# Kernel tuning notes

Measured on AMD Instinct MI355X. Metric: run time of the kernel, lower is better.

The kernel has to match this reference:

```python
import jax, jax.numpy as jnp
import numpy as np

N = 1024
C_LOCAL = 384
C_PAIR = 128
HEADS = 8
KEY_SIZE = 32
LN_EPS = 1e-5


def setup_inputs() -> dict:
    key = jax.random.key(0)
    ks = jax.random.split(key, 5)
    local = jax.random.normal(ks[0], (N, C_LOCAL), dtype=jnp.float32)
    pair = jax.random.normal(ks[1], (N, N, C_PAIR), dtype=jnp.float32)
    mask = jnp.ones((N,), dtype=bool)
    ln_scale = jnp.ones((C_LOCAL,), dtype=jnp.float32)
    ln_offset = jnp.zeros((C_LOCAL,), dtype=jnp.float32)
    W_value = jax.random.normal(ks[2], (C_LOCAL, HEADS * KEY_SIZE), dtype=jnp.float32) * (1.0 / np.sqrt(C_LOCAL))
    W_attn = jax.random.normal(ks[3], (C_PAIR, HEADS), dtype=jnp.float32) * (1.0 / np.sqrt(C_PAIR))
    W_out = jax.random.normal(ks[4], (HEADS * KEY_SIZE, C_LOCAL), dtype=jnp.float32) * (1.0 / np.sqrt(HEADS * KEY_SIZE))
    return {"local": local, "pair": pair, "mask": mask,
            "ln_scale": ln_scale, "ln_offset": ln_offset,
            "W_value": W_value, "W_attn": W_attn, "W_out": W_out}


def reference(local, pair, mask, ln_scale, ln_offset, W_value, W_attn, W_out):
    # pair_mask[i, j] = mask[i] & mask[j]
    pair_mask = (mask[:, None] & mask[None, :])[..., None]  # [N, N, 1]

    # LayerNorm over last axis (create_scale=True, create_offset=True)
    mu = jnp.mean(local, axis=-1, keepdims=True)
    var = jnp.var(local, axis=-1, keepdims=True)
    local_ln = (local - mu) * jax.lax.rsqrt(var + LN_EPS) * ln_scale + ln_offset

    # value projection -> [N, heads, key_size]
    value = (local_ln @ W_value).reshape(local.shape[0], HEADS, KEY_SIZE)

    # pair-bias attention logits -> [N, N, heads]
    attn = pair @ W_attn
    attn = jnp.where(pair_mask, attn, -1e9)
    attn = jax.nn.softmax(attn, axis=1)
    attn = jnp.where(pair_mask, attn, 0.0)

    # weighted average over j, per head -> [N, heads, key_size] -> [N, heads*key_size]
    out = jnp.einsum('ijh,jhc->ihc', attn, value).reshape(local.shape[0], -1)
    return out @ W_out
```

## Files before the change

### kernel.cpp

```cpp
#include <hip/hip_runtime.h>
#include <cstddef>

#define NN 1024
#define CL 384
#define CP 128
#define NH 8
#define KS 32
#define HK 256

typedef float floatx4 __attribute__((ext_vector_type(4)));

template<int CTRL>
__device__ __forceinline__ float dpp_mov(float v) {
    return __int_as_float(__builtin_amdgcn_update_dpp(
        0, __float_as_int(v), CTRL, 0xF, 0xF, true));
}

__device__ __forceinline__ float4 ntload4(const float* p) {
    floatx4 t = __builtin_nontemporal_load((const floatx4*)p);
    float4 r; r.x = t.x; r.y = t.y; r.z = t.z; r.w = t.w;
    return r;
}

__global__ __launch_bounds__(256) void k_ln_value(
    const float* __restrict__ local_, const float* __restrict__ ln_scale,
    const float* __restrict__ ln_offset, const float* __restrict__ Wv,
    float* __restrict__ value)
{
    __shared__ float ln_s[4][CL];
    const int tid = threadIdx.x;
    const int w = tid >> 6, lane = tid & 63;
    const int r = blockIdx.x * 4 + w;
    const float* lp = local_ + (size_t)r * CL;
    float x[6]; float s1 = 0.f, s2 = 0.f;
#pragma unroll
    for (int k = 0; k < 6; ++k) { x[k] = lp[lane + 64*k]; s1 += x[k]; s2 += x[k]*x[k]; }
#pragma unroll
    for (int m = 1; m < 64; m <<= 1) { s1 += __shfl_xor(s1, m); s2 += __shfl_xor(s2, m); }
    const float mean = s1 * (1.f/CL);
    const float var  = fmaxf(s2 * (1.f/CL) - mean*mean, 0.f);
    const float rstd = rsqrtf(var + 1e-5f);
#pragma unroll
    for (int k = 0; k < 6; ++k) {
        const int c = lane + 64*k;
        ln_s[w][c] = (x[k]-mean)*rstd*ln_scale[c] + ln_offset[c];
    }
    __syncthreads();
    const int m_ = tid;
    float acc0=0.f, acc1=0.f, acc2=0.f, acc3=0.f;
    for (int c0 = 0; c0 < CL; c0 += 8) {
        float wv[8];
#pragma unroll
        for (int cc = 0; cc < 8; ++cc) wv[cc] = Wv[(size_t)(c0+cc)*HK + m_];
        {
            const float4 a = *(const float4*)&ln_s[0][c0];
            const float4 b = *(const float4*)&ln_s[0][c0+4];
            acc0 += a.x*wv[0]+a.y*wv[1]+a.z*wv[2]+a.w*wv[3]+b.x*wv[4]+b.y*wv[5]+b.z*wv[6]+b.w*wv[7];
        }
        {
            const float4 a = *(const float4*)&ln_s[1][c0];
            const float4 b = *(const float4*)&ln_s[1][c0+4];
            acc1 += a.x*wv[0]+a.y*wv[1]+a.z*wv[2]+a.w*wv[3]+b.x*wv[4]+b.y*wv[5]+b.z*wv[6]+b.w*wv[7];
        }
        {
            const float4 a = *(const float4*)&ln_s[2][c0];
            const float4 b = *(const float4*)&ln_s[2][c0+4];
            acc2 += a.x*wv[0]+a.y*wv[1]+a.z*wv[2]+a.w*wv[3]+b.x*wv[4]+b.y*wv[5]+b.z*wv[6]+b.w*wv[7];
        }
        {
            const float4 a = *(const float4*)&ln_s[3][c0];
            const float4 b = *(const float4*)&ln_s[3][c0+4];
            acc3 += a.x*wv[0]+a.y*wv[1]+a.z*wv[2]+a.w*wv[3]+b.x*wv[4]+b.y*wv[5]+b.z*wv[6]+b.w*wv[7];
        }
    }
    const int rb = blockIdx.x*4;
    value[(size_t)(rb+0)*HK + m_] = acc0;
    value[(size_t)(rb+1)*HK + m_] = acc1;
    value[(size_t)(rb+2)*HK + m_] = acc2;
    value[(size_t)(rb+3)*HK + m_] = acc3;
}

__global__ __launch_bounds__(256, 4) void k_attn(
    const float* __restrict__ pair, const int* __restrict__ mask,
    const float* __restrict__ Wa, const float* __restrict__ value,
    const float* __restrict__ Wo, float* __restrict__ outp)
{
    __shared__ float zf[NN];
    __shared__ float sep[4][NH];
    __shared__ float ov4[4][64][4];
    __shared__ float ov[HK];

    const int tid  = threadIdx.x;
    const int w    = tid >> 6;
    const int lane = tid & 63;
    const int sub5 = lane & 31;
    const int half = lane >> 5;
    const int i = blockIdx.x;
    const bool bmi = mask[i] != 0;

    for (int k = tid; k < NN; k += 256)
        zf[k] = (bmi && (mask[k] != 0)) ? 1.f : 0.f;

    float wreg[32];
    {
        const float4* wp = (const float4*)(Wa + sub5*4*NH);
#pragma unroll
        for (int k = 0; k < 8; ++k) {
            const float4 t4 = wp[k];
            wreg[4*k+0]=t4.x; wreg[4*k+1]=t4.y; wreg[4*k+2]=t4.z; wreg[4*k+3]=t4.w;
        }
    }

    const int hpv  = lane >> 3;
    const int srcE = ((hpv>>2)&1) + 2*((hpv>>1)&1) + 8*(hpv&1);
    const int srcO = srcE + 32;

    const int jbase = w * 256;
    const float* pb = pair + (size_t)i*NN*CP + sub5*4;

    float4 ac4; ac4.x = ac4.y = ac4.z = ac4.w = 0.f;
    float se_loc = 0.f;

    float4 cur[4], nxt[4];
#pragma unroll
    for (int s = 0; s < 4; ++s)
        cur[s] = ntload4(pb + (size_t)(jbase + 2*s + half)*CP);

    __syncthreads();

    for (int t = 0; t < 32; ++t) {
        const int j0 = jbase + t*8;
        const int jp = jbase + (((t+1)&31)*8);
#pragma unroll
        for (int s = 0; s < 4; ++s)
            nxt[s] = ntload4(pb + (size_t)(jp + 2*s + half)*CP);

#pragma unroll
        for (int s = 0; s < 4; ++s) {
            const float4 c = cur[s];
            float acc[8];
#pragma unroll
            for (int h = 0; h < 8; ++h)
                acc[h] = c.x*wreg[h] + c.y*wreg[8+h] + c.z*wreg[16+h] + c.w*wreg[24+h];
            const bool b0 = (sub5 & 1) != 0;
            const bool b1 = (sub5 & 2) != 0;
            const bool b3 = (sub5 & 8) != 0;
            float r4[4];
#pragma unroll
            for (int k = 0; k < 4; ++k)
                r4[k] = (b0 ? acc[k+4] : acc[k]) + dpp_mov<0xB1>(b0 ? acc[k] : acc[k+4]);
            float r2[2];
#pragma unroll
            for (int k = 0; k < 2; ++k)
                r2[k] = (b1 ? r4[k+2] : r4[k]) + dpp_mov<0x4E>(b1 ? r4[k] : r4[k+2]);
            float r1 = (b3 ? r2[1] : r2[0]) + dpp_mov<0x128>(b3 ? r2[0] : r2[1]);
            r1 += __shfl_xor(r1, 4);
            r1 += __shfl_xor(r1, 16);
            const float pe = __expf(r1);
            const float p_e = __shfl(pe, srcE) * zf[j0 + 2*s];
            const float p_o = __shfl(pe, srcO) * zf[j0 + 2*s + 1];
            se_loc += p_e + p_o;
            const float* vb = value + (size_t)(j0 + 2*s)*HK + lane*4;
            const float4 ve = *(const float4*)vb;
            const float4 vo = *(const float4*)(vb + HK);
            ac4.x += p_e*ve.x + p_o*vo.x;
            ac4.y += p_e*ve.y + p_o*vo.y;
            ac4.z += p_e*ve.z + p_o*vo.z;
            ac4.w += p_e*ve.w + p_o*vo.w;
        }
#pragma unroll
        for (int s = 0; s < 4; ++s) cur[s] = nxt[s];
    }

    if ((lane & 7) == 0) sep[w][hpv] = se_loc;
    ov4[w][lane][0] = ac4.x; ov4[w][lane][1] = ac4.y;
    ov4[w][lane][2] = ac4.z; ov4[w][lane][3] = ac4.w;
    __syncthreads();

    {
        const int m = tid;
        const float s4 = ov4[0][m>>2][m&3] + ov4[1][m>>2][m&3]
                       + ov4[2][m>>2][m&3] + ov4[3][m>>2][m&3];
        const int h = m >> 5;
        const float se = sep[0][h] + sep[1][h] + sep[2][h] + sep[3][h];
        const float inv = (se > 0.f) ? (1.f/se) : 0.f;
        ov[m] = s4 * inv;
    }
    __syncthreads();

    for (int o = tid; o < CL; o += 256) {
        float a0 = 0.f;
        for (int m = 0; m < HK; m += 4) {
            const float4 x0 = *(const float4*)&ov[m];
            a0 += x0.x*Wo[(size_t)(m+0)*CL + o] + x0.y*Wo[(size_t)(m+1)*CL + o]
                + x0.z*Wo[(size_t)(m+2)*CL + o] + x0.w*Wo[(size_t)(m+3)*CL + o];
        }
        outp[(size_t)i*CL + o] = a0;
    }
}

extern "C" void kernel_launch(void* const* d_in, const int* in_sizes, int n_in,
                              void* d_out, int out_size, void* d_ws, size_t ws_size,
                              hipStream_t stream)
{
    (void)in_sizes; (void)n_in; (void)out_size; (void)ws_size;
    const float* local_ = (const float*)d_in[0];
    const float* pair   = (const float*)d_in[1];
    const int*   mask   = (const int*)d_in[2];
    const float* scale  = (const float*)d_in[3];
    const float* offset = (const float*)d_in[4];
    const float* Wv     = (const float*)d_in[5];
    const float* Wa     = (const float*)d_in[6];
    const float* Wo     = (const float*)d_in[7];
    float* value = (float*)d_ws;
    k_ln_value<<<NN/4, 256, 0, stream>>>(local_, scale, offset, Wv, value);
    k_attn<<<NN, 256, 0, stream>>>(pair, mask, Wa, value, Wo, (float*)d_out);
}
```

Measured before the change: 154.9 us.

## Deepen pair-tensor prefetch to two stages and batch value loads early

The attention loop now keeps two register buffers of pair rows in flight, prefetching two iterations ahead instead of one, and reissues each buffer's load right after its logits are computed. Value rows for the whole 8-row step are loaded up front so their latency overlaps the logit math. This aims to hide more HBM latency on the streamed pair tensor, at the cost of extra VGPRs that may reduce occupancy under the 4-blocks-per-SM launch bound.

```diff
diff --git a/kernel.cpp b/kernel.cpp
--- a/kernel.cpp
+++ b/kernel.cpp
@@ -121,56 +121,81 @@
     float4 ac4; ac4.x = ac4.y = ac4.z = ac4.w = 0.f;
     float se_loc = 0.f;
 
-    float4 cur[4], nxt[4];
+    float4 pA[4], pB[4];
 #pragma unroll
     for (int s = 0; s < 4; ++s)
-        cur[s] = ntload4(pb + (size_t)(jbase + 2*s + half)*CP);
-
-    __syncthreads();
-
-    for (int t = 0; t < 32; ++t) {
-        const int j0 = jbase + t*8;
-        const int jp = jbase + (((t+1)&31)*8);
-#pragma unroll
-        for (int s = 0; s < 4; ++s)
-            nxt[s] = ntload4(pb + (size_t)(jp + 2*s + half)*CP);
-
-#pragma unroll
-        for (int s = 0; s < 4; ++s) {
-            const float4 c = cur[s];
-            float acc[8];
-#pragma unroll
-            for (int h = 0; h < 8; ++h)
-                acc[h] = c.x*wreg[h] + c.y*wreg[8+h] + c.z*wreg[16+h] + c.w*wreg[24+h];
-            const bool b0 = (sub5 & 1) != 0;
-            const bool b1 = (sub5 & 2) != 0;
-            const bool b3 = (sub5 & 8) != 0;
-            float r4[4];
-#pragma unroll
-            for (int k = 0; k < 4; ++k)
-                r4[k] = (b0 ? acc[k+4] : acc[k]) + dpp_mov<0xB1>(b0 ? acc[k] : acc[k+4]);
-            float r2[2];
-#pragma unroll
-            for (int k = 0; k < 2; ++k)
-                r2[k] = (b1 ? r4[k+2] : r4[k]) + dpp_mov<0x4E>(b1 ? r4[k] : r4[k+2]);
-            float r1 = (b3 ? r2[1] : r2[0]) + dpp_mov<0x128>(b3 ? r2[0] : r2[1]);
-            r1 += __shfl_xor(r1, 4);
-            r1 += __shfl_xor(r1, 16);
-            const float pe = __expf(r1);
-            const float p_e = __shfl(pe, srcE) * zf[j0 + 2*s];
-            const float p_o = __shfl(pe, srcO) * zf[j0 + 2*s + 1];
-            se_loc += p_e + p_o;
-            const float* vb = value + (size_t)(j0 + 2*s)*HK + lane*4;
-            const float4 ve = *(const float4*)vb;
-            const float4 vo = *(const float4*)(vb + HK);
-            ac4.x += p_e*ve.x + p_o*vo.x;
-            ac4.y += p_e*ve.y + p_o*vo.y;
-            ac4.z += p_e*ve.z + p_o*vo.z;
-            ac4.w += p_e*ve.w + p_o*vo.w;
-        }
-#pragma unroll
-        for (int s = 0; s < 4; ++s) cur[s] = nxt[s];
-    }
+        pA[s] = ntload4(pb + (size_t)(jbase + 2*s + half)*CP);
+#pragma unroll
+    for (int s = 0; s < 4; ++s)
+        pB[s] = ntload4(pb + (size_t)(jbase + 8 + 2*s + half)*CP);
+
+    __syncthreads();
+
+#define ITER(BUF, T)                                                          \
+    {                                                                         \
+        const int j0 = jbase + (T)*8;                                         \
+        const int jp = jbase + ((((T)+2)&31)*8);                              \
+                                           \
+        float4 ve[4], vo[4];                                                  \
+        {                                                                     \
+            const float* vb0 = value + (size_t)j0*HK + lane*4;                \
+            _Pragma("unroll")                                                 \
+            for (int s = 0; s < 4; ++s) {                                     \
+                ve[s] = *(const float4*)(vb0 + (size_t)(2*s)*HK);             \
+                vo[s] = *(const float4*)(vb0 + (size_t)(2*s+1)*HK);           \
+            }                                                                 \
+        }                                                                     \
+                                \
+        float pe[4];                                                          \
+        _Pragma("unroll")                                                     \
+        for (int s = 0; s < 4; ++s) {                                         \
+            const float4 c = BUF[s];                                          \
+            float acc[8];                                                     \
+            _Pragma("unroll")                                                 \
+            for (int h = 0; h < 8; ++h)                                       \
+                acc[h] = c.x*wreg[h] + c.y*wreg[8+h]                          \
+                       + c.z*wreg[16+h] + c.w*wreg[24+h];                     \
+            const bool b0 = (sub5 & 1) != 0;                                  \
+            const bool b1 = (sub5 & 2) != 0;                                  \
+            const bool b3 = (sub5 & 8) != 0;                                  \
+            float r4[4];                                                      \
+            _Pragma("unroll")                                                 \
+            for (int k = 0; k < 4; ++k)                                       \
+                r4[k] = (b0 ? acc[k+4] : acc[k])                              \
+                      + dpp_mov<0xB1>(b0 ? acc[k] : acc[k+4]);                \
+            float r2[2];                                                      \
+            _Pragma("unroll")                                                 \
+            for (int k = 0; k < 2; ++k)                                       \
+                r2[k] = (b1 ? r4[k+2] : r4[k])                                \
+                      + dpp_mov<0x4E>(b1 ? r4[k] : r4[k+2]);                  \
+            float r1 = (b3 ? r2[1] : r2[0])                                   \
+                     + dpp_mov<0x128>(b3 ? r2[0] : r2[1]);                    \
+            r1 += __shfl_xor(r1, 4);                                          \
+            r1 += __shfl_xor(r1, 16);                                         \
+            pe[s] = __expf(r1);                                               \
+        }                                                                     \
+                         \
+        _Pragma("unroll")                                                     \
+        for (int s = 0; s < 4; ++s)                                           \
+            BUF[s] = ntload4(pb + (size_t)(jp + 2*s + half)*CP);              \
+                           \
+        _Pragma("unroll")                                                     \
+        for (int s = 0; s < 4; ++s) {                                         \
+            const float p_e = __shfl(pe[s], srcE) * zf[j0 + 2*s];             \
+            const float p_o = __shfl(pe[s], srcO) * zf[j0 + 2*s + 1];         \
+            se_loc += p_e + p_o;                                              \
+            ac4.x += p_e*ve[s].x + p_o*vo[s].x;                               \
+            ac4.y += p_e*ve[s].y + p_o*vo[s].y;                               \
+            ac4.z += p_e*ve[s].z + p_o*vo[s].z;                               \
+            ac4.w += p_e*ve[s].w + p_o*vo[s].w;                               \
+        }                                                                     \
+    }
+
+    for (int t = 0; t < 32; t += 2) {
+        ITER(pA, t);
+        ITER(pB, t+1);
+    }
+#undef ITER
 
     if ((lane & 7) == 0) sep[w][hpv] = se_loc;
     ov4[w][lane][0] = ac4.x; ov4[w][lane][1] = ac4.y;
```

Result: slower. 204.3 us (+31.9%).

## Use fp16 MFMA for pair-bias logits and packed fp16 values with fdot2

Applied to the files above, without the earlier changes.

Replaces the per-lane FMA plus DPP reduction for the pair@W_attn logits with 16x16x32 fp16 MFMA on converted pair tiles. Stores the value projection as packed fp16 pairs of adjacent rows and accumulates the weighted sum with fdot2. The double-buffered pair load now fetches 16 rows per step, and the occupancy hint drops from 4 to 3. The aim is to cut the VALU and shuffle cost so the kernel is limited by the pair stream. In exchange it adds fp16 rounding error in the logits, probabilities and values.

```diff
diff --git a/kernel.cpp b/kernel.cpp
--- a/kernel.cpp
+++ b/kernel.cpp
@@ -9,12 +9,12 @@
 #define HK 256
 
 typedef float floatx4 __attribute__((ext_vector_type(4)));
-
-template<int CTRL>
-__device__ __forceinline__ float dpp_mov(float v) {
-    return __int_as_float(__builtin_amdgcn_update_dpp(
-        0, __float_as_int(v), CTRL, 0xF, 0xF, true));
-}
+typedef float f32x4 __attribute__((ext_vector_type(4)));
+typedef __fp16 f16x8 __attribute__((ext_vector_type(8)));
+typedef __fp16 f16x2 __attribute__((ext_vector_type(2)));
+
+union H8 { f16x8 v; f16x2 h[4]; };
+union HU { unsigned u; f16x2 h; };
 
 __device__ __forceinline__ float4 ntload4(const float* p) {
     floatx4 t = __builtin_nontemporal_load((const floatx4*)p);
@@ -25,7 +25,7 @@
 __global__ __launch_bounds__(256) void k_ln_value(
     const float* __restrict__ local_, const float* __restrict__ ln_scale,
     const float* __restrict__ ln_offset, const float* __restrict__ Wv,
-    float* __restrict__ value)
+    unsigned* __restrict__ vp)
 {
     __shared__ float ln_s[4][CL];
     const int tid = threadIdx.x;
@@ -73,106 +73,125 @@
             acc3 += a.x*wv[0]+a.y*wv[1]+a.z*wv[2]+a.w*wv[3]+b.x*wv[4]+b.y*wv[5]+b.z*wv[6]+b.w*wv[7];
         }
     }
-    const int rb = blockIdx.x*4;
-    value[(size_t)(rb+0)*HK + m_] = acc0;
-    value[(size_t)(rb+1)*HK + m_] = acc1;
-    value[(size_t)(rb+2)*HK + m_] = acc2;
-    value[(size_t)(rb+3)*HK + m_] = acc3;
-}
-
-__global__ __launch_bounds__(256, 4) void k_attn(
+    const int rb2 = blockIdx.x*2;
+    HU pa, pb;
+    pa.h = __builtin_amdgcn_cvt_pkrtz(acc0, acc1);
+    pb.h = __builtin_amdgcn_cvt_pkrtz(acc2, acc3);
+    vp[(size_t)(rb2+0)*HK + m_] = pa.u;
+    vp[(size_t)(rb2+1)*HK + m_] = pb.u;
+}
+
+__global__ __launch_bounds__(256, 3) void k_attn(
     const float* __restrict__ pair, const int* __restrict__ mask,
-    const float* __restrict__ Wa, const float* __restrict__ value,
+    const float* __restrict__ Wa, const unsigned* __restrict__ vp,
     const float* __restrict__ Wo, float* __restrict__ outp)
 {
     __shared__ float zf[NN];
-    __shared__ float sep[4][NH];
+    __shared__ float sew[4][NH];
     __shared__ float ov4[4][64][4];
     __shared__ float ov[HK];
 
     const int tid  = threadIdx.x;
     const int w    = tid >> 6;
     const int lane = tid & 63;
-    const int sub5 = lane & 31;
-    const int half = lane >> 5;
+    const int n15  = lane & 15;
+    const int kg   = lane >> 4;
+    const int hq   = lane >> 3;
     const int i = blockIdx.x;
     const bool bmi = mask[i] != 0;
 
     for (int k = tid; k < NN; k += 256)
         zf[k] = (bmi && (mask[k] != 0)) ? 1.f : 0.f;
 
-    float wreg[32];
-    {
-        const float4* wp = (const float4*)(Wa + sub5*4*NH);
-#pragma unroll
-        for (int k = 0; k < 8; ++k) {
-            const float4 t4 = wp[k];
-            wreg[4*k+0]=t4.x; wreg[4*k+1]=t4.y; wreg[4*k+2]=t4.z; wreg[4*k+3]=t4.w;
-        }
-    }
-
-    const int hpv  = lane >> 3;
-    const int srcE = ((hpv>>2)&1) + 2*((hpv>>1)&1) + 8*(hpv&1);
-    const int srcO = srcE + 32;
+    f16x8 bf[4];
+#pragma unroll
+    for (int ks = 0; ks < 4; ++ks) {
+        H8 u;
+#pragma unroll
+        for (int d = 0; d < 4; ++d) {
+            const int k0 = ks*KS + kg*8 + 2*d;
+            const float e0 = (n15 < NH) ? Wa[(size_t)k0*NH + n15] : 0.f;
+            const float e1 = (n15 < NH) ? Wa[(size_t)(k0+1)*NH + n15] : 0.f;
+            u.h[d] = __builtin_amdgcn_cvt_pkrtz(e0, e1);
+        }
+        bf[ks] = u.v;
+    }
 
     const int jbase = w * 256;
-    const float* pb = pair + (size_t)i*NN*CP + sub5*4;
+    const float* abase = pair + (size_t)i*NN*CP + (size_t)n15*CP + kg*8;
+
+    float4 Aa[8], Ab[8];
+    auto LOADA = [&](float4* d, int j0) {
+#pragma unroll
+        for (int ks = 0; ks < 4; ++ks) {
+            const float* b = abase + (size_t)j0*CP + ks*KS;
+            d[2*ks]   = ntload4(b);
+            d[2*ks+1] = ntload4(b + 4);
+        }
+    };
 
     float4 ac4; ac4.x = ac4.y = ac4.z = ac4.w = 0.f;
     float se_loc = 0.f;
 
-    float4 cur[4], nxt[4];
-#pragma unroll
-    for (int s = 0; s < 4; ++s)
-        cur[s] = ntload4(pb + (size_t)(jbase + 2*s + half)*CP);
-
-    __syncthreads();
-
-    for (int t = 0; t < 32; ++t) {
-        const int j0 = jbase + t*8;
-        const int jp = jbase + (((t+1)&31)*8);
-#pragma unroll
-        for (int s = 0; s < 4; ++s)
-            nxt[s] = ntload4(pb + (size_t)(jp + 2*s + half)*CP);
-
-#pragma unroll
-        for (int s = 0; s < 4; ++s) {
-            const float4 c = cur[s];
-            float acc[8];
-#pragma unroll
-            for (int h = 0; h < 8; ++h)
-                acc[h] = c.x*wreg[h] + c.y*wreg[8+h] + c.z*wreg[16+h] + c.w*wreg[24+h];
-            const bool b0 = (sub5 & 1) != 0;
-            const bool b1 = (sub5 & 2) != 0;
-            const bool b3 = (sub5 & 8) != 0;
-            float r4[4];
-#pragma unroll
-            for (int k = 0; k < 4; ++k)
-                r4[k] = (b0 ? acc[k+4] : acc[k]) + dpp_mov<0xB1>(b0 ? acc[k] : acc[k+4]);
-            float r2[2];
-#pragma unroll
-            for (int k = 0; k < 2; ++k)
-                r2[k] = (b1 ? r4[k+2] : r4[k]) + dpp_mov<0x4E>(b1 ? r4[k] : r4[k+2]);
-            float r1 = (b3 ? r2[1] : r2[0]) + dpp_mov<0x128>(b3 ? r2[0] : r2[1]);
-            r1 += __shfl_xor(r1, 4);
-            r1 += __shfl_xor(r1, 16);
-            const float pe = __expf(r1);
-            const float p_e = __shfl(pe, srcE) * zf[j0 + 2*s];
-            const float p_o = __shfl(pe, srcO) * zf[j0 + 2*s + 1];
-            se_loc += p_e + p_o;
-            const float* vb = value + (size_t)(j0 + 2*s)*HK + lane*4;
-            const float4 ve = *(const float4*)vb;
-            const float4 vo = *(const float4*)(vb + HK);
-            ac4.x += p_e*ve.x + p_o*vo.x;
-            ac4.y += p_e*ve.y + p_o*vo.y;
-            ac4.z += p_e*ve.z + p_o*vo.z;
-            ac4.w += p_e*ve.w + p_o*vo.w;
-        }
-#pragma unroll
-        for (int s = 0; s < 4; ++s) cur[s] = nxt[s];
-    }
-
-    if ((lane & 7) == 0) sep[w][hpv] = se_loc;
+    LOADA(Aa, jbase);
+    LOADA(Ab, jbase + 16);
+    __syncthreads();
+
+    auto ITER = [&](float4* BUF, int T) {
+        const int j0 = jbase + T*16;
+        uint4 vv[8];
+        {
+            const unsigned* vb = vp + (size_t)(j0 >> 1)*HK + lane*4;
+#pragma unroll
+            for (int pr = 0; pr < 8; ++pr)
+                vv[pr] = *(const uint4*)(vb + (size_t)pr*HK);
+        }
+        f16x8 fr[4];
+#pragma unroll
+        for (int ks = 0; ks < 4; ++ks) {
+            H8 u;
+            u.h[0] = __builtin_amdgcn_cvt_pkrtz(BUF[2*ks].x,   BUF[2*ks].y);
+            u.h[1] = __builtin_amdgcn_cvt_pkrtz(BUF[2*ks].z,   BUF[2*ks].w);
+            u.h[2] = __builtin_amdgcn_cvt_pkrtz(BUF[2*ks+1].x, BUF[2*ks+1].y);
+            u.h[3] = __builtin_amdgcn_cvt_pkrtz(BUF[2*ks+1].z, BUF[2*ks+1].w);
+            fr[ks] = u.v;
+        }
+        if (T + 2 < 16) LOADA(BUF, jbase + (T+2)*16);
+        f32x4 acc = {0.f, 0.f, 0.f, 0.f};
+#pragma unroll
+        for (int ks = 0; ks < 4; ++ks)
+            acc = __builtin_amdgcn_mfma_f32_16x16x32_f16(fr[ks], bf[ks], acc, 0, 0, 0);
+        float pe[4];
+#pragma unroll
+        for (int r = 0; r < 4; ++r)
+            pe[r] = zf[j0 + kg*4 + r] * __expf(acc[r]);
+        se_loc += pe[0] + pe[1] + pe[2] + pe[3];
+#pragma unroll
+        for (int pr = 0; pr < 8; ++pr) {
+            const int src = (pr >> 1)*16 + hq;
+            const float p0 = __shfl(pe[2*(pr & 1)],     src);
+            const float p1 = __shfl(pe[2*(pr & 1) + 1], src);
+            const f16x2 ppk = __builtin_amdgcn_cvt_pkrtz(p0, p1);
+            HU d0, d1, d2, d3;
+            d0.u = vv[pr].x; d1.u = vv[pr].y; d2.u = vv[pr].z; d3.u = vv[pr].w;
+            ac4.x = __builtin_amdgcn_fdot2(ppk, d0.h, ac4.x, false);
+            ac4.y = __builtin_amdgcn_fdot2(ppk, d1.h, ac4.y, false);
+            ac4.z = __builtin_amdgcn_fdot2(ppk, d2.h, ac4.z, false);
+            ac4.w = __builtin_amdgcn_fdot2(ppk, d3.h, ac4.w, false);
+        }
+    };
+
+    for (int t = 0; t < 16; t += 2) {
+        ITER(Aa, t);
+        ITER(Ab, t + 1);
+    }
+
+    {
+        float se_t = se_loc;
+        se_t += __shfl_xor(se_t, 16);
+        se_t += __shfl_xor(se_t, 32);
+        if (lane < NH) sew[w][lane] = se_t;
+    }
     ov4[w][lane][0] = ac4.x; ov4[w][lane][1] = ac4.y;
     ov4[w][lane][2] = ac4.z; ov4[w][lane][3] = ac4.w;
     __syncthreads();
@@ -182,7 +201,7 @@
         const float s4 = ov4[0][m>>2][m&3] + ov4[1][m>>2][m&3]
                        + ov4[2][m>>2][m&3] + ov4[3][m>>2][m&3];
         const int h = m >> 5;
-        const float se = sep[0][h] + sep[1][h] + sep[2][h] + sep[3][h];
+        const float se = sew[0][h] + sew[1][h] + sew[2][h] + sew[3][h];
         const float inv = (se > 0.f) ? (1.f/se) : 0.f;
         ov[m] = s4 * inv;
     }
@@ -212,7 +231,7 @@
     const float* Wv     = (const float*)d_in[5];
     const float* Wa     = (const float*)d_in[6];
     const float* Wo     = (const float*)d_in[7];
-    float* value = (float*)d_ws;
-    k_ln_value<<<NN/4, 256, 0, stream>>>(local_, scale, offset, Wv, value);
-    k_attn<<<NN, 256, 0, stream>>>(pair, mask, Wa, value, Wo, (float*)d_out);
-}
+    unsigned* vp = (unsigned*)d_ws;
+    k_ln_value<<<NN/4, 256, 0, stream>>>(local_, scale, offset, Wv, vp);
+    k_attn<<<NN, 256, 0, stream>>>(pair, mask, Wa, vp, Wo, (float*)d_out);
+}
```

New measurement: 304.3 us. 1.96x slower.
